# Kernel tuning notes

Hardware: AMD Instinct MI355X
Metric: run time of the kernel (lower is better)

The kernel has to match this reference:

```python
import jax, jax.numpy as jnp
import numpy as np

N_ENTS = 50000
N_RELS = 500
EMB = 256
N_LAYERS = 2
N_EDGES = 400000
BATCH = 512
BN_EPS = 1e-5


def make_quaternion_mul(kernel):
    # kernel: [m, 4*dim] -> hamilton: [4*m, 4*dim]
    r, i, j, k = jnp.split(kernel, 4, axis=1)
    r2 = jnp.concatenate([r, -i, -j, -k], axis=0)
    i2 = jnp.concatenate([i, r, -k, j], axis=0)
    j2 = jnp.concatenate([j, k, r, -i], axis=0)
    k2 = jnp.concatenate([k, -j, i, r], axis=0)
    return jnp.concatenate([r2, i2, j2, k2], axis=1)


def batchnorm(x, gamma, beta):
    mean = jnp.mean(x, axis=0)
    var = jnp.var(x, axis=0)  # biased, as torch BN training normalization
    return (x - mean) * jax.lax.rsqrt(var + BN_EPS) * gamma + beta


def q4gnn_layer(X, rows, cols, vals, W, gamma, beta, n_nodes):
    hamilton = make_quaternion_mul(W)          # [d, d]
    support = X @ hamilton                     # [n, d]
    agg = jax.ops.segment_sum(vals[:, None] * support[cols], rows, num_segments=n_nodes)
    return jnp.tanh(batchnorm(agg, gamma, beta))


def vec_vec_wise_multiplication(q, p):
    # quaternion componentwise-normalized hamilton product; q, p: [B, d]
    d = q.shape[1]
    size = d // 4
    pn = p.reshape(-1, 4, size)
    pn = pn / jnp.sqrt(jnp.sum(pn * pn, axis=1, keepdims=True))
    pn = pn.reshape(-1, d)
    qr, qi, qj, qk = jnp.split(q, 4, axis=1)
    q_r = jnp.concatenate([qr, -qi, -qj, -qk], axis=1)
    q_i = jnp.concatenate([qi, qr, -qk, qj], axis=1)
    q_j = jnp.concatenate([qj, qk, qr, -qi], axis=1)
    q_k = jnp.concatenate([qk, -qj, qi, qr], axis=1)
    def qwise(x):
        return jnp.sum((x * pn).reshape(-1, 4, size), axis=1)
    return jnp.concatenate([qwise(q_r), qwise(q_i), qwise(q_j), qwise(q_k)], axis=1)


def quate_score(h, r, X, gamma, beta):
    hr = vec_vec_wise_multiplication(h, r)
    hr = batchnorm(hr, gamma, beta)            # dropout = identity (eval)
    return hr @ X.T                            # [B, n_ents]


def setup_inputs() -> dict:
    key = jax.random.key(0)
    ks = jax.random.split(key, 12)
    return {
        "e1_idx": jax.random.randint(ks[0], (BATCH,), 0, N_ENTS),
        "r_idx": jax.random.randint(ks[1], (BATCH,), 0, N_RELS),
        "embeddings": jax.random.normal(ks[2], (N_ENTS + N_RELS, EMB), jnp.float32) * 0.1,
        "gcn1_w": jax.random.normal(ks[3], (N_LAYERS, EMB // 4, EMB), jnp.float32) * 0.1,
        "gcn2_w": jax.random.normal(ks[4], (N_LAYERS, EMB // 4, EMB), jnp.float32) * 0.1,
        "gcn1_gamma": jnp.ones((N_LAYERS, EMB), jnp.float32),
        "gcn1_beta": jnp.zeros((N_LAYERS, EMB), jnp.float32),
        "gcn2_gamma": jnp.ones((N_LAYERS, EMB), jnp.float32),
        "gcn2_beta": jnp.zeros((N_LAYERS, EMB), jnp.float32),
        "lin_ents": jax.random.normal(ks[5], (N_LAYERS, EMB // 2, EMB), jnp.float32) * 0.1,
        "bn_s_gamma": jnp.ones((3, EMB), jnp.float32),
        "bn_s_beta": jnp.zeros((3, EMB), jnp.float32),
        "adj_rows": jax.random.randint(ks[6], (N_EDGES,), 0, N_ENTS),
        "adj_cols": jax.random.randint(ks[7], (N_EDGES,), 0, N_ENTS),
        "adj_vals": jax.random.uniform(ks[8], (N_EDGES,), jnp.float32),
        "adjr_rows": jax.random.randint(ks[9], (N_EDGES,), 0, N_ENTS + N_RELS),
        "adjr_cols": jax.random.randint(ks[10], (N_EDGES,), 0, N_ENTS + N_RELS),
        "adjr_vals": jax.random.uniform(ks[11], (N_EDGES,), jnp.float32),
    }


def reference(e1_idx, r_idx, embeddings, gcn1_w, gcn2_w, gcn1_gamma, gcn1_beta,
              gcn2_gamma, gcn2_beta, lin_ents, bn_s_gamma, bn_s_beta,
              adj_rows, adj_cols, adj_vals, adjr_rows, adjr_cols, adjr_vals):
    X = embeddings[:N_ENTS]
    R = embeddings[N_ENTS:]
    scores = [jax.nn.sigmoid(quate_score(X[e1_idx], R[r_idx], X, bn_s_gamma[0], bn_s_beta[0]))]
    for l in range(N_LAYERS):
        XR = jnp.concatenate([X, R], axis=0)
        XRrf = q4gnn_layer(XR, adjr_rows, adjr_cols, adjr_vals,
                           gcn2_w[l], gcn2_gamma[l], gcn2_beta[l], N_ENTS + N_RELS)
        Xef = q4gnn_layer(X, adj_rows, adj_cols, adj_vals,
                          gcn1_w[l], gcn1_gamma[l], gcn1_beta[l], N_ENTS)
        Xrf = XRrf[:N_ENTS]
        # combine_type == 'cat': interleave quaternion components -> [N, 2*EMB]
        e1, e2, e3, e4 = jnp.split(Xef, 4, axis=1)
        r1, r2, r3, r4 = jnp.split(Xrf, 4, axis=1)
        Xcat = jnp.concatenate([e1, r1, e2, r2, e3, r3, e4, r4], axis=1)
        X = Xcat @ make_quaternion_mul(lin_ents[l])  # [N, EMB]
        R = XRrf[N_ENTS:]
        scores.append(jax.nn.sigmoid(
            quate_score(X[e1_idx], R[r_idx], X, bn_s_gamma[l + 1], bn_s_beta[l + 1])))
    return jnp.stack(scores)  # [N_LAYERS+1, B, N_ENTS]
```

## Files before the change

kernel.cpp:

```cpp
#include <hip/hip_runtime.h>
#include <math.h>

#define N_ENTS 50000
#define N_RELS 500
#define N_ALL  50500
#define EMB    256
#define NEDGE  400000
#define BATCH  512
#define BN_EPS 1e-5f

typedef unsigned short u16;
typedef unsigned int   u32;
typedef __attribute__((ext_vector_type(8))) short s16x8;
typedef __attribute__((ext_vector_type(4))) float f32x4;

#define LSTR 40

__device__ __forceinline__ u16 f2b(float x) {
    u32 u = __float_as_uint(x);
    return (u16)((u + 0x7fffu + ((u >> 16) & 1u)) >> 16);
}
__device__ __forceinline__ float b2f(u16 h) {
    return __uint_as_float((u32)h << 16);
}

__global__ __launch_bounds__(256) void split_kernel(
    const float* __restrict__ x, u16* __restrict__ hi, u16* __restrict__ lo,
    long n4) {
    long i = (long)blockIdx.x * 256 + threadIdx.x;
    if (i >= n4) return;
    float4 v = ((const float4*)x)[i];
    u16 h0 = f2b(v.x), h1 = f2b(v.y), h2 = f2b(v.z), h3 = f2b(v.w);
    u16 l0 = f2b(v.x - b2f(h0)), l1 = f2b(v.y - b2f(h1));
    u16 l2 = f2b(v.z - b2f(h2)), l3 = f2b(v.w - b2f(h3));
    uint2 hp, lp;
    hp.x = (u32)h0 | ((u32)h1 << 16); hp.y = (u32)h2 | ((u32)h3 << 16);
    lp.x = (u32)l0 | ((u32)l1 << 16); lp.y = (u32)l2 | ((u32)l3 << 16);
    ((uint2*)hi)[i] = hp;
    ((uint2*)lo)[i] = lp;
}

__global__ __launch_bounds__(256) void build_ht_kernel(
    const float* __restrict__ W, u16* __restrict__ Hhi, u16* __restrict__ Hlo,
    int P) {
    int K4 = 4 * P;
    int idx = blockIdx.x * 256 + threadIdx.x;
    int total = 256 * K4;
    if (idx >= total) return;
    int n = idx / K4, k = idx - n * K4;
    int a = k / P, p = k - a * P;
    int c = n >> 6, s = n & 63;
    const int  comp[4][4] = {{0,1,2,3},{1,0,3,2},{2,3,0,1},{3,2,1,0}};
    const float sgn[4][4] = {{1.f,1.f,1.f,1.f},
                             {-1.f,1.f,1.f,-1.f},
                             {-1.f,-1.f,1.f,1.f},
                             {-1.f,1.f,-1.f,1.f}};
    float v = sgn[a][c] * W[p * 256 + comp[a][c] * 64 + s];
    u16 h = f2b(v);
    Hhi[idx] = h;
    Hlo[idx] = f2b(v - b2f(h));
}

__global__ __launch_bounds__(256) void bn_coeff_kernel(
    const float* __restrict__ stats, int n, const float* __restrict__ gamma,
    const float* __restrict__ beta, float2* __restrict__ coef) {
    int col = threadIdx.x;
    float inv_n = 1.f / (float)n;
    float mean = stats[col] * inv_n;
    float var = stats[256 + col] * inv_n - mean * mean;
    float sc = rsqrtf(var + BN_EPS) * gamma[col];
    coef[col] = make_float2(sc, beta[col] - mean * sc);
}

template <int ROWS>
__device__ __forceinline__ void stage_rows(
    const u16* __restrict__ Shi, const u16* __restrict__ Slo,
    long row0, int rows_left, int K, int k0,
    u16* __restrict__ Lh, u16* __restrict__ Ll, int tid) {
#pragma unroll
    for (int p = 0; p < ROWS / 64; p++) {
        int idx = tid + p * 256;
        int r = idx >> 2, c = idx & 3;
        uint4 vh = make_uint4(0, 0, 0, 0), vl = make_uint4(0, 0, 0, 0);
        if (r < rows_left) {
            long base = (row0 + r) * (long)K + k0 + c * 8;
            vh = *(const uint4*)&Shi[base];
            vl = *(const uint4*)&Slo[base];
        }
        *(uint4*)&Lh[r * LSTR + c * 8] = vh;
        *(uint4*)&Ll[r * LSTR + c * 8] = vl;
    }
}

__device__ __forceinline__ void stage_f32_split(
    const float* __restrict__ S, long row0, int rows_left, int K, int k0,
    u16* __restrict__ Lh, u16* __restrict__ Ll, int tid) {
#pragma unroll
    for (int p = 0; p < 4; p++) {
        int idx = tid + p * 256;
        int r = idx >> 3, c4 = idx & 7;
        float4 v = make_float4(0.f, 0.f, 0.f, 0.f);
        if (r < rows_left)
            v = *(const float4*)&S[(row0 + r) * (long)K + k0 + c4 * 4];
        u16 h0 = f2b(v.x), h1 = f2b(v.y), h2 = f2b(v.z), h3 = f2b(v.w);
        u16 l0 = f2b(v.x - b2f(h0)), l1 = f2b(v.y - b2f(h1));
        u16 l2 = f2b(v.z - b2f(h2)), l3 = f2b(v.w - b2f(h3));
        uint2 hp, lp;
        hp.x = (u32)h0 | ((u32)h1 << 16); hp.y = (u32)h2 | ((u32)h3 << 16);
        lp.x = (u32)l0 | ((u32)l1 << 16); lp.y = (u32)l2 | ((u32)l3 << 16);
        *(uint2*)&Lh[r * LSTR + c4 * 4] = hp;
        *(uint2*)&Ll[r * LSTR + c4 * 4] = lp;
    }
}

__device__ __forceinline__ void mfma_tile256(
    const u16* __restrict__ Ah, const u16* __restrict__ Al,
    const u16* __restrict__ Bh, const u16* __restrict__ Bl,
    int wm, int wn, int lane, f32x4 acc[4][8]) {
    int lr = lane & 15, kg = lane >> 4;
    s16x8 ah[4], al[4];
#pragma unroll
    for (int fm = 0; fm < 4; fm++) {
        int off = (wm + fm * 16 + lr) * LSTR + kg * 8;
        ah[fm] = *(const s16x8*)&Ah[off];
        al[fm] = *(const s16x8*)&Al[off];
    }
#pragma unroll
    for (int fn = 0; fn < 8; fn++) {
        int off = (wn + fn * 16 + lr) * LSTR + kg * 8;
        s16x8 bh = *(const s16x8*)&Bh[off];
        s16x8 bl = *(const s16x8*)&Bl[off];
#pragma unroll
        for (int fm = 0; fm < 4; fm++) {
            acc[fm][fn] = __builtin_amdgcn_mfma_f32_16x16x32_bf16(
                ah[fm], bh, acc[fm][fn], 0, 0, 0);
            acc[fm][fn] = __builtin_amdgcn_mfma_f32_16x16x32_bf16(
                ah[fm], bl, acc[fm][fn], 0, 0, 0);
            acc[fm][fn] = __builtin_amdgcn_mfma_f32_16x16x32_bf16(
                al[fm], bh, acc[fm][fn], 0, 0, 0);
        }
    }
}

__global__ __launch_bounds__(256, 2) void mfma_agg_kernel(
    const float* __restrict__ G,
    const u16* __restrict__ Bhi, const u16* __restrict__ Blo,
    float* __restrict__ C, float* __restrict__ stats, int M) {
    __shared__ u16 Ah[128 * LSTR], Al[128 * LSTR];
    __shared__ u16 Bh[256 * LSTR], Bl[256 * LSTR];
    int tid = threadIdx.x, lane = tid & 63, wid = tid >> 6;
    int wm = (wid >> 1) * 64, wn = (wid & 1) * 128;
    long bm0 = (long)blockIdx.y * 128;
    int rA = (int)(((long)M - bm0 < 128) ? (long)M - bm0 : 128);
    f32x4 acc[4][8] = {};
    for (int k0 = 0; k0 < 256; k0 += 32) {
        if (k0) __syncthreads();
        stage_f32_split(G, bm0, rA, 256, k0, Ah, Al, tid);
        stage_rows<256>(Bhi, Blo, 0, 256, 256, k0, Bh, Bl, tid);
        __syncthreads();
        mfma_tile256(Ah, Al, Bh, Bl, wm, wn, lane, acc);
    }
    int lr = lane & 15, lq = lane >> 4;
#pragma unroll
    for (int fm = 0; fm < 4; fm++) {
#pragma unroll
        for (int r = 0; r < 4; r++) {
            long row = bm0 + wm + fm * 16 + lq * 4 + r;
            if (row < M) {
#pragma unroll
                for (int fn = 0; fn < 8; fn++) {
                    long col = wn + fn * 16 + lr;
                    C[row * 256 + col] = acc[fm][fn][r];
                }
            }
        }
    }
#pragma unroll
    for (int fn = 0; fn < 8; fn++) {
        float s = 0.f, sq = 0.f;
#pragma unroll
        for (int fm = 0; fm < 4; fm++)
#pragma unroll
            for (int r = 0; r < 4; r++) {
                float v = acc[fm][fn][r];
                s += v;
                sq += v * v;
            }
        s += __shfl_xor(s, 16);  s += __shfl_xor(s, 32);
        sq += __shfl_xor(sq, 16); sq += __shfl_xor(sq, 32);
        if (lane < 16) {
            int col = wn + fn * 16 + lr;
            atomicAdd(&stats[col], s);
            atomicAdd(&stats[256 + col], sq);
        }
    }
}

__global__ __launch_bounds__(256, 2) void mfma_score_kernel(
    const u16* __restrict__ Ahi, const u16* __restrict__ Alo,
    const u16* __restrict__ Bhi, const u16* __restrict__ Blo,
    float* __restrict__ out) {
    __shared__ u16 Ah[128 * LSTR], Al[128 * LSTR];
    __shared__ u16 Bh[256 * LSTR], Bl[256 * LSTR];
    int tid = threadIdx.x, lane = tid & 63, wid = tid >> 6;
    int wm = (wid >> 1) * 64, wn = (wid & 1) * 128;
    long bm0 = (long)blockIdx.y * 128, bn0 = (long)blockIdx.x * 256;
    int rB = (int)(((long)N_ENTS - bn0 < 256) ? (long)N_ENTS - bn0 : 256);
    f32x4 acc[4][8] = {};
    for (int k0 = 0; k0 < 256; k0 += 32) {
        if (k0) __syncthreads();
        stage_rows<128>(Ahi, Alo, bm0, 128, 256, k0, Ah, Al, tid);
        stage_rows<256>(Bhi, Blo, bn0, rB, 256, k0, Bh, Bl, tid);
        __syncthreads();
        mfma_tile256(Ah, Al, Bh, Bl, wm, wn, lane, acc);
    }
    int lr = lane & 15, lq = lane >> 4;
#pragma unroll
    for (int fm = 0; fm < 4; fm++) {
#pragma unroll
        for (int r = 0; r < 4; r++) {
            long row = bm0 + wm + fm * 16 + lq * 4 + r;
#pragma unroll
            for (int fn = 0; fn < 8; fn++) {
                long col = bn0 + wn + fn * 16 + lr;
                if (col < N_ENTS) {
                    float v = acc[fm][fn][r];
                    out[row * N_ENTS + col] = 1.f / (1.f + __expf(-v));
                }
            }
        }
    }
}

__global__ __launch_bounds__(256, 2) void mfma_lin_kernel(
    const float* __restrict__ Xef, const float* __restrict__ Xrf,
    const float2* __restrict__ coefE, const float2* __restrict__ coefR,
    const u16* __restrict__ Bhi, const u16* __restrict__ Blo,
    u16* __restrict__ Chi, u16* __restrict__ Clo, int M) {
    __shared__ u16 Ah[128 * LSTR], Al[128 * LSTR];
    __shared__ u16 Bh[256 * LSTR], Bl[256 * LSTR];
    int tid = threadIdx.x, lane = tid & 63, wid = tid >> 6;
    int wm = (wid >> 1) * 64, wn = (wid & 1) * 128;
    int bm0 = blockIdx.y * 128;
    f32x4 acc[4][8] = {};
    for (int k0 = 0; k0 < 512; k0 += 32) {
        if (k0) __syncthreads();
#pragma unroll
        for (int p = 0; p < 4; p++) {
            int idx = tid + p * 256;
            int r = idx >> 3, c4 = idx & 7;
            int kk = k0 + c4 * 4;
            int chunk = kk >> 6, s = kk & 63;
            int gm = bm0 + r;
            const float* src = (chunk & 1) ? Xrf : Xef;
            const float2* cf = (chunk & 1) ? coefR : coefE;
            int base = (chunk >> 1) * 64 + s;
            float4 v = make_float4(0.f, 0.f, 0.f, 0.f);
            if (gm < M) v = *(const float4*)&src[(long)gm * 256 + base];
            float2 c0 = cf[base], c1 = cf[base + 1];
            float2 c2 = cf[base + 2], c3 = cf[base + 3];
            v.x = tanhf(fmaf(v.x, c0.x, c0.y));
            v.y = tanhf(fmaf(v.y, c1.x, c1.y));
            v.z = tanhf(fmaf(v.z, c2.x, c2.y));
            v.w = tanhf(fmaf(v.w, c3.x, c3.y));
            u16 h0 = f2b(v.x), h1 = f2b(v.y), h2 = f2b(v.z), h3 = f2b(v.w);
            u16 l0 = f2b(v.x - b2f(h0)), l1 = f2b(v.y - b2f(h1));
            u16 l2 = f2b(v.z - b2f(h2)), l3 = f2b(v.w - b2f(h3));
            uint2 hp, lp;
            hp.x = (u32)h0 | ((u32)h1 << 16); hp.y = (u32)h2 | ((u32)h3 << 16);
            lp.x = (u32)l0 | ((u32)l1 << 16); lp.y = (u32)l2 | ((u32)l3 << 16);
            *(uint2*)&Ah[r * LSTR + c4 * 4] = hp;
            *(uint2*)&Al[r * LSTR + c4 * 4] = lp;
        }
        stage_rows<256>(Bhi, Blo, 0, 256, 512, k0, Bh, Bl, tid);
        __syncthreads();
        mfma_tile256(Ah, Al, Bh, Bl, wm, wn, lane, acc);
    }
    int lr = lane & 15, lq = lane >> 4;
#pragma unroll
    for (int fm = 0; fm < 4; fm++) {
#pragma unroll
        for (int r = 0; r < 4; r++) {
            long row = (long)bm0 + wm + fm * 16 + lq * 4 + r;
            if (row < M) {
#pragma unroll
                for (int fn = 0; fn < 8; fn++) {
                    long col = wn + fn * 16 + lr;
                    float v = acc[fm][fn][r];
                    u16 h = f2b(v);
                    Chi[row * 256 + col] = h;
                    Clo[row * 256 + col] = f2b(v - b2f(h));
                }
            }
        }
    }
}

__global__ __launch_bounds__(256) void hist_kernel(
    const int* __restrict__ rows, int* __restrict__ cnt, int n_edges) {
    int e = blockIdx.x * 256 + threadIdx.x;
    if (e < n_edges) atomicAdd(&cnt[rows[e]], 1);
}

__global__ __launch_bounds__(1024) void exscan_kernel(
    const int* __restrict__ cnt, int n, int* __restrict__ off) {
    __shared__ int part[1024];
    int t = threadIdx.x;
    int chunk = (n + 1023) / 1024;
    int lo = t * chunk;
    int hi = lo + chunk; if (hi > n) hi = n;
    int s = 0;
    for (int i = lo; i < hi; i++) s += cnt[i];
    part[t] = s;
    __syncthreads();
    for (int d = 1; d < 1024; d <<= 1) {
        int v = (t >= d) ? part[t - d] : 0;
        __syncthreads();
        part[t] += v;
        __syncthreads();
    }
    int base = (t == 0) ? 0 : part[t - 1];
    for (int i = lo; i < hi; i++) {
        off[i] = base;
        base += cnt[i];
    }
    if (hi >= n) off[n] = base;
}

__global__ __launch_bounds__(256) void scatter_kernel(
    const int* __restrict__ rows, const int* __restrict__ cols,
    const float* __restrict__ vals, int* __restrict__ cursor,
    int2* __restrict__ pack, int n_edges) {
    int e = blockIdx.x * 256 + threadIdx.x;
    if (e >= n_edges) return;
    int r = rows[e];
    int p = atomicAdd(&cursor[r], 1);
    pack[p] = make_int2(cols[e], __float_as_int(vals[e]));
}

__global__ __launch_bounds__(256) void csr_gather_kernel(
    const u16* __restrict__ xhi, const u16* __restrict__ xlo,
    const int* __restrict__ off, const int2* __restrict__ pack,
    float* __restrict__ G, int n_rows) {
    int gid = blockIdx.x * 256 + threadIdx.x;
    int row = gid >> 6;
    int lane = gid & 63;
    if (row >= n_rows) return;
    int beg = off[row], end = off[row + 1];
    float4 acc = {0.f, 0.f, 0.f, 0.f};
    int e = beg;
    for (; e + 4 <= end; e += 4) {
        int2 cv0 = pack[e], cv1 = pack[e + 1], cv2 = pack[e + 2], cv3 = pack[e + 3];
        long b0 = (long)cv0.x * 256 + lane * 4;
        long b1 = (long)cv1.x * 256 + lane * 4;
        long b2 = (long)cv2.x * 256 + lane * 4;
        long b3 = (long)cv3.x * 256 + lane * 4;
        uint2 h0 = *(const uint2*)(xhi + b0), l0 = *(const uint2*)(xlo + b0);
        uint2 h1 = *(const uint2*)(xhi + b1), l1 = *(const uint2*)(xlo + b1);
        uint2 h2 = *(const uint2*)(xhi + b2), l2 = *(const uint2*)(xlo + b2);
        uint2 h3 = *(const uint2*)(xhi + b3), l3 = *(const uint2*)(xlo + b3);
        float v0 = __int_as_float(cv0.y), v1 = __int_as_float(cv1.y);
        float v2 = __int_as_float(cv2.y), v3 = __int_as_float(cv3.y);
        acc.x = fmaf(v0, b2f((u16)(h0.x & 0xffff)) + b2f((u16)(l0.x & 0xffff)), acc.x);
        acc.y = fmaf(v0, b2f((u16)(h0.x >> 16))    + b2f((u16)(l0.x >> 16)),    acc.y);
        acc.z = fmaf(v0, b2f((u16)(h0.y & 0xffff)) + b2f((u16)(l0.y & 0xffff)), acc.z);
        acc.w = fmaf(v0, b2f((u16)(h0.y >> 16))    + b2f((u16)(l0.y >> 16)),    acc.w);
        acc.x = fmaf(v1, b2f((u16)(h1.x & 0xffff)) + b2f((u16)(l1.x & 0xffff)), acc.x);
        acc.y = fmaf(v1, b2f((u16)(h1.x >> 16))    + b2f((u16)(l1.x >> 16)),    acc.y);
        acc.z = fmaf(v1, b2f((u16)(h1.y & 0xffff)) + b2f((u16)(l1.y & 0xffff)), acc.z);
        acc.w = fmaf(v1, b2f((u16)(h1.y >> 16))    + b2f((u16)(l1.y >> 16)),    acc.w);
        acc.x = fmaf(v2, b2f((u16)(h2.x & 0xffff)) + b2f((u16)(l2.x & 0xffff)), acc.x);
        acc.y = fmaf(v2, b2f((u16)(h2.x >> 16))    + b2f((u16)(l2.x >> 16)),    acc.y);
        acc.z = fmaf(v2, b2f((u16)(h2.y & 0xffff)) + b2f((u16)(l2.y & 0xffff)), acc.z);
        acc.w = fmaf(v2, b2f((u16)(h2.y >> 16))    + b2f((u16)(l2.y >> 16)),    acc.w);
        acc.x = fmaf(v3, b2f((u16)(h3.x & 0xffff)) + b2f((u16)(l3.x & 0xffff)), acc.x);
        acc.y = fmaf(v3, b2f((u16)(h3.x >> 16))    + b2f((u16)(l3.x >> 16)),    acc.y);
        acc.z = fmaf(v3, b2f((u16)(h3.y & 0xffff)) + b2f((u16)(l3.y & 0xffff)), acc.z);
        acc.w = fmaf(v3, b2f((u16)(h3.y >> 16))    + b2f((u16)(l3.y >> 16)),    acc.w);
    }
    for (; e < end; e++) {
        int2 cv = pack[e];
        float v = __int_as_float(cv.y);
        long b = (long)cv.x * 256 + lane * 4;
        uint2 hv = *(const uint2*)(xhi + b), lv = *(const uint2*)(xlo + b);
        acc.x = fmaf(v, b2f((u16)(hv.x & 0xffff)) + b2f((u16)(lv.x & 0xffff)), acc.x);
        acc.y = fmaf(v, b2f((u16)(hv.x >> 16))    + b2f((u16)(lv.x >> 16)),    acc.y);
        acc.z = fmaf(v, b2f((u16)(hv.y & 0xffff)) + b2f((u16)(lv.y & 0xffff)), acc.z);
        acc.w = fmaf(v, b2f((u16)(hv.y >> 16))    + b2f((u16)(lv.y >> 16)),    acc.w);
    }
    *(float4*)(G + (long)row * 256 + lane * 4) = acc;
}

__global__ __launch_bounds__(256) void bn_stats_kernel(
    const float* __restrict__ x, int n, float* __restrict__ stats) {
    int col = threadIdx.x;
    int r0 = blockIdx.x * 256;
    int r1 = r0 + 256;
    if (r1 > n) r1 = n;
    float s = 0.f, sq = 0.f;
    for (int r = r0; r < r1; r++) {
        float v = x[(long)r * 256 + col];
        s += v;
        sq += v * v;
    }
    atomicAdd(&stats[col], s);
    atomicAdd(&stats[256 + col], sq);
}

__global__ __launch_bounds__(256) void bn_apply_split_kernel(
    const float* __restrict__ x, u16* __restrict__ hi, u16* __restrict__ lo,
    int n, const float* __restrict__ gamma, const float* __restrict__ beta,
    const float* __restrict__ stats) {
    long total = (long)n * 256;
    float inv_n = 1.f / (float)n;
    long idx = (long)blockIdx.x * 256 + threadIdx.x;
    if (idx >= total) return;
    int col = (int)(idx & 255);
    float mean = stats[col] * inv_n;
    float var = stats[256 + col] * inv_n - mean * mean;
    float sc = rsqrtf(var + BN_EPS) * gamma[col];
    float v = (x[idx] - mean) * sc + beta[col];
    u16 h = f2b(v);
    hi[idx] = h;
    lo[idx] = f2b(v - b2f(h));
}

__global__ __launch_bounds__(256) void bn_tanh_split_kernel(
    const float* __restrict__ x, const float2* __restrict__ coef,
    u16* __restrict__ hi, u16* __restrict__ lo, long total) {
    long idx = (long)blockIdx.x * 256 + threadIdx.x;
    if (idx >= total) return;
    int col = (int)(idx & 255);
    float2 c = coef[col];
    float v = tanhf(fmaf(x[idx], c.x, c.y));
    u16 h = f2b(v);
    hi[idx] = h;
    lo[idx] = f2b(v - b2f(h));
}

__global__ __launch_bounds__(256) void hr_kernel(
    const u16* __restrict__ xhi, const u16* __restrict__ xlo,
    const int* __restrict__ e1_idx, const int* __restrict__ r_idx,
    float* __restrict__ hr) {
    int idx = blockIdx.x * 256 + threadIdx.x;
    if (idx >= BATCH * 64) return;
    int b = idx >> 6, s = idx & 63;
    long hrow = (long)e1_idx[b] * 256;
    long prow = ((long)N_ENTS + r_idx[b]) * 256;
    float qr = b2f(xhi[hrow + s])       + b2f(xlo[hrow + s]);
    float qi = b2f(xhi[hrow + 64 + s])  + b2f(xlo[hrow + 64 + s]);
    float qj = b2f(xhi[hrow + 128 + s]) + b2f(xlo[hrow + 128 + s]);
    float qk = b2f(xhi[hrow + 192 + s]) + b2f(xlo[hrow + 192 + s]);
    float pr = b2f(xhi[prow + s])       + b2f(xlo[prow + s]);
    float pi = b2f(xhi[prow + 64 + s])  + b2f(xlo[prow + 64 + s]);
    float pj = b2f(xhi[prow + 128 + s]) + b2f(xlo[prow + 128 + s]);
    float pk = b2f(xhi[prow + 192 + s]) + b2f(xlo[prow + 192 + s]);
    float inv = rsqrtf(pr * pr + pi * pi + pj * pj + pk * pk);
    pr *= inv; pi *= inv; pj *= inv; pk *= inv;
    float* o = hr + (long)b * 256 + s;
    o[0]   = qr * pr - qi * pi - qj * pj - qk * pk;
    o[64]  = qi * pr + qr * pi - qk * pj + qj * pk;
    o[128] = qj * pr + qk * pi + qr * pj - qi * pk;
    o[192] = qk * pr - qj * pi + qi * pj + qr * pk;
}

struct Csr {
    int* off;
    int* cur;
    int2* pack;
};

struct Ws {
    float* Gbuf;
    float* aggA;
    float* aggB;
    float* hr;
    float* statsHr;
    float* statsA;
    float* statsB;
    float2* coefA;
    float2* coefB;
    u16* xr_hi;
    u16* xr_lo;
    u16* hrn_hi;
    u16* hrn_lo;
    u16* ht_hi;
    u16* ht_lo;
    Csr adj;
    Csr adjr;
};

static void build_csr(const int* rows, const int* cols, const float* vals,
                      int n_rows, const Csr& c, hipStream_t stream) {
    hipMemsetAsync(c.cur, 0, (size_t)n_rows * sizeof(int), stream);
    hist_kernel<<<(NEDGE + 255) / 256, 256, 0, stream>>>(rows, c.cur, NEDGE);
    exscan_kernel<<<1, 1024, 0, stream>>>(c.cur, n_rows, c.off);
    hipMemcpyAsync(c.cur, c.off, (size_t)n_rows * sizeof(int),
                   hipMemcpyDeviceToDevice, stream);
    scatter_kernel<<<(NEDGE + 255) / 256, 256, 0, stream>>>(
        rows, cols, vals, c.cur, c.pack, NEDGE);
}

static void run_split(const float* x, u16* hi, u16* lo, long n,
                      hipStream_t stream) {
    long n4 = n / 4;
    split_kernel<<<(int)((n4 + 255) / 256), 256, 0, stream>>>(x, hi, lo, n4);
}

static void run_q4gnn(int n, const Csr& c, const float* W,
                      const float* gamma, const float* beta,
                      float* agg, float* stats, float2* coef,
                      const Ws& w, hipStream_t stream) {
    hipMemsetAsync(stats, 0, 512 * sizeof(float), stream);
    int gblocks = (n * 64 + 255) / 256;
    csr_gather_kernel<<<gblocks, 256, 0, stream>>>(
        w.xr_hi, w.xr_lo, c.off, c.pack, w.Gbuf, n);
    build_ht_kernel<<<(256 * 256) / 256, 256, 0, stream>>>(W, w.ht_hi, w.ht_lo, 64);
    dim3 g(1, (n + 127) / 128);
    mfma_agg_kernel<<<g, 256, 0, stream>>>(w.Gbuf, w.ht_hi, w.ht_lo, agg, stats, n);
    bn_coeff_kernel<<<1, 256, 0, stream>>>(stats, n, gamma, beta, coef);
}

static void run_score(const int* e1_idx, const int* r_idx, const float* gamma,
                      const float* beta, float* out_l, const Ws& w,
                      hipStream_t stream) {
    hr_kernel<<<(BATCH * 64) / 256, 256, 0, stream>>>(
        w.xr_hi, w.xr_lo, e1_idx, r_idx, w.hr);
    hipMemsetAsync(w.statsHr, 0, 512 * sizeof(float), stream);
    bn_stats_kernel<<<(BATCH + 255) / 256, 256, 0, stream>>>(w.hr, BATCH, w.statsHr);
    bn_apply_split_kernel<<<(BATCH * 256) / 256, 256, 0, stream>>>(
        w.hr, w.hrn_hi, w.hrn_lo, BATCH, gamma, beta, w.statsHr);
    dim3 g((N_ENTS + 255) / 256, BATCH / 128);
    mfma_score_kernel<<<g, 256, 0, stream>>>(
        w.hrn_hi, w.hrn_lo, w.xr_hi, w.xr_lo, out_l);
}

extern "C" void kernel_launch(void* const* d_in, const int* in_sizes, int n_in,
                              void* d_out, int out_size, void* d_ws, size_t ws_size,
                              hipStream_t stream) {
    const int*   e1_idx     = (const int*)d_in[0];
    const int*   r_idx      = (const int*)d_in[1];
    const float* emb        = (const float*)d_in[2];
    const float* gcn1_w     = (const float*)d_in[3];
    const float* gcn2_w     = (const float*)d_in[4];
    const float* gcn1_gamma = (const float*)d_in[5];
    const float* gcn1_beta  = (const float*)d_in[6];
    const float* gcn2_gamma = (const float*)d_in[7];
    const float* gcn2_beta  = (const float*)d_in[8];
    const float* lin_ents   = (const float*)d_in[9];
    const float* bn_s_gamma = (const float*)d_in[10];
    const float* bn_s_beta  = (const float*)d_in[11];
    const int*   adj_rows   = (const int*)d_in[12];
    const int*   adj_cols   = (const int*)d_in[13];
    const float* adj_vals   = (const float*)d_in[14];
    const int*   adjr_rows  = (const int*)d_in[15];
    const int*   adjr_cols  = (const int*)d_in[16];
    const float* adjr_vals  = (const float*)d_in[17];
    float* out = (float*)d_out;

    Ws w;
    float* f = (float*)d_ws;
    w.Gbuf       = f; f += (long)N_ALL * EMB;
    w.aggA       = f; f += (long)N_ALL * EMB;
    w.aggB       = f; f += (long)N_ENTS * EMB;
    w.hr         = f; f += BATCH * EMB;
    w.statsHr    = f; f += 512;
    w.statsA     = f; f += 512;
    w.statsB     = f; f += 512;
    w.coefA      = (float2*)f; f += 512;
    w.coefB      = (float2*)f; f += 512;
    w.xr_hi  = (u16*)f; f += (long)N_ALL * EMB / 2;
    w.xr_lo  = (u16*)f; f += (long)N_ALL * EMB / 2;
    w.hrn_hi = (u16*)f; f += BATCH * EMB / 2;
    w.hrn_lo = (u16*)f; f += BATCH * EMB / 2;
    w.ht_hi  = (u16*)f; f += 256 * 512 / 2;
    w.ht_lo  = (u16*)f; f += 256 * 512 / 2;
    int* ip = (int*)f;
    w.adj.pack  = (int2*)ip; ip += 2 * NEDGE;
    w.adjr.pack = (int2*)ip; ip += 2 * NEDGE;
    w.adj.off    = ip; ip += N_ENTS + 1;
    w.adj.cur    = ip; ip += N_ENTS;
    w.adjr.off   = ip; ip += N_ALL + 1;
    w.adjr.cur   = ip; ip += N_ALL;

    build_csr(adj_rows, adj_cols, adj_vals, N_ENTS, w.adj, stream);
    build_csr(adjr_rows, adjr_cols, adjr_vals, N_ALL, w.adjr, stream);

    run_split(emb, w.xr_hi, w.xr_lo, (long)N_ALL * EMB, stream);

    run_score(e1_idx, r_idx, bn_s_gamma, bn_s_beta, out, w, stream);

    for (int l = 0; l < 2; l++) {
        run_q4gnn(N_ALL, w.adjr, gcn2_w + (long)l * 64 * 256,
                  gcn2_gamma + l * 256, gcn2_beta + l * 256,
                  w.aggA, w.statsA, w.coefA, w, stream);
        run_q4gnn(N_ENTS, w.adj, gcn1_w + (long)l * 64 * 256,
                  gcn1_gamma + l * 256, gcn1_beta + l * 256,
                  w.aggB, w.statsB, w.coefB, w, stream);
        build_ht_kernel<<<(256 * 512) / 256, 256, 0, stream>>>(
            lin_ents + (long)l * 128 * 256, w.ht_hi, w.ht_lo, 128);
        dim3 g(1, (N_ENTS + 127) / 128);
        mfma_lin_kernel<<<g, 256, 0, stream>>>(
            w.aggB, w.aggA, w.coefB, w.coefA, w.ht_hi, w.ht_lo,
            w.xr_hi, w.xr_lo, N_ENTS);
        bn_tanh_split_kernel<<<(N_RELS * EMB + 255) / 256, 256, 0, stream>>>(
            w.aggA + (long)N_ENTS * EMB, w.coefA,
            w.xr_hi + (long)N_ENTS * EMB, w.xr_lo + (long)N_ENTS * EMB,
            (long)N_RELS * EMB);
        run_score(e1_idx, r_idx, bn_s_gamma + (l + 1) * 256,
                  bn_s_beta + (l + 1) * 256,
                  out + (long)(l + 1) * BATCH * N_ENTS, w, stream);
    }
}
```

Measured before the change: 1.667 ms.

## Batch both GNN branches into shared gather/GEMM launches and remap score blocks

The two q4gnn branches (relation graph and entity graph) now run their CSR gathers in one combined launch and their Hamilton GEMMs in one combined launch, with separate gather buffers and Hamilton matrices so neither branch overwrites the other. This cuts the number of launches and fills the GPU better, especially for the small tail grids. The score GEMM now uses a 1D grid whose block index is remapped so that consecutive blocks spread across groups of eight, which changes which blocks run together and which B tiles they share in cache. It costs an extra gather buffer and one more Hamilton buffer in workspace.

After: 1.634 ms. 1.02x faster.

```diff
diff --git a/kernel.cpp b/kernel.cpp
--- a/kernel.cpp
+++ b/kernel.cpp
@@ -142,21 +142,32 @@
     }
 }
 
-__global__ __launch_bounds__(256, 2) void mfma_agg_kernel(
-    const float* __restrict__ G,
-    const u16* __restrict__ Bhi, const u16* __restrict__ Blo,
-    float* __restrict__ C, float* __restrict__ stats, int M) {
+__global__ __launch_bounds__(256, 2) void mfma_agg2_kernel(
+    const float* __restrict__ GA, const float* __restrict__ GB,
+    const u16* __restrict__ AhiB, const u16* __restrict__ AloB,
+    const u16* __restrict__ BhiB, const u16* __restrict__ BloB,
+    float* __restrict__ CA, float* __restrict__ CB,
+    float* __restrict__ statsA, float* __restrict__ statsB, int tA) {
     __shared__ u16 Ah[128 * LSTR], Al[128 * LSTR];
     __shared__ u16 Bh[256 * LSTR], Bl[256 * LSTR];
     int tid = threadIdx.x, lane = tid & 63, wid = tid >> 6;
     int wm = (wid >> 1) * 64, wn = (wid & 1) * 128;
-    long bm0 = (long)blockIdx.y * 128;
+    int by = blockIdx.y;
+    const float* G; const u16* Hhi; const u16* Hlo;
+    float* C; float* stats; int M; long bm0;
+    if (by < tA) {
+        G = GA; Hhi = AhiB; Hlo = AloB; C = CA; stats = statsA;
+        M = N_ALL; bm0 = (long)by * 128;
+    } else {
+        G = GB; Hhi = BhiB; Hlo = BloB; C = CB; stats = statsB;
+        M = N_ENTS; bm0 = (long)(by - tA) * 128;
+    }
     int rA = (int)(((long)M - bm0 < 128) ? (long)M - bm0 : 128);
     f32x4 acc[4][8] = {};
     for (int k0 = 0; k0 < 256; k0 += 32) {
         if (k0) __syncthreads();
         stage_f32_split(G, bm0, rA, 256, k0, Ah, Al, tid);
-        stage_rows<256>(Bhi, Blo, 0, 256, 256, k0, Bh, Bl, tid);
+        stage_rows<256>(Hhi, Hlo, 0, 256, 256, k0, Bh, Bl, tid);
         __syncthreads();
         mfma_tile256(Ah, Al, Bh, Bl, wm, wn, lane, acc);
     }
@@ -204,7 +215,10 @@
     __shared__ u16 Bh[256 * LSTR], Bl[256 * LSTR];
     int tid = threadIdx.x, lane = tid & 63, wid = tid >> 6;
     int wm = (wid >> 1) * 64, wn = (wid & 1) * 128;
-    long bm0 = (long)blockIdx.y * 128, bn0 = (long)blockIdx.x * 256;
+    int b = blockIdx.x;
+    int w = (b & 7) * 98 + (b >> 3);
+    long bm0 = (long)(w & 3) * 128;
+    long bn0 = (long)(w >> 2) * 256;
     int rB = (int)(((long)N_ENTS - bn0 < 256) ? (long)N_ENTS - bn0 : 256);
     f32x4 acc[4][8] = {};
     for (int k0 = 0; k0 < 256; k0 += 32) {
@@ -338,15 +352,23 @@
     pack[p] = make_int2(cols[e], __float_as_int(vals[e]));
 }
 
-__global__ __launch_bounds__(256) void csr_gather_kernel(
+__global__ __launch_bounds__(256) void csr_gather2_kernel(
     const u16* __restrict__ xhi, const u16* __restrict__ xlo,
-    const int* __restrict__ off, const int2* __restrict__ pack,
-    float* __restrict__ G, int n_rows) {
+    const int* __restrict__ offA, const int2* __restrict__ packA,
+    const int* __restrict__ offB, const int2* __restrict__ packB,
+    float* __restrict__ GA, float* __restrict__ GB, int nA, int nB) {
     int gid = blockIdx.x * 256 + threadIdx.x;
     int row = gid >> 6;
     int lane = gid & 63;
-    if (row >= n_rows) return;
-    int beg = off[row], end = off[row + 1];
+    const int* off; const int2* pack; float* G; int r;
+    if (row < nA) {
+        off = offA; pack = packA; G = GA; r = row;
+    } else {
+        r = row - nA;
+        if (r >= nB) return;
+        off = offB; pack = packB; G = GB;
+    }
+    int beg = off[r], end = off[r + 1];
     float4 acc = {0.f, 0.f, 0.f, 0.f};
     int e = beg;
     for (; e + 4 <= end; e += 4) {
@@ -388,7 +410,7 @@
         acc.z = fmaf(v, b2f((u16)(hv.y & 0xffff)) + b2f((u16)(lv.y & 0xffff)), acc.z);
         acc.w = fmaf(v, b2f((u16)(hv.y >> 16))    + b2f((u16)(lv.y >> 16)),    acc.w);
     }
-    *(float4*)(G + (long)row * 256 + lane * 4) = acc;
+    *(float4*)(G + (long)r * 256 + lane * 4) = acc;
 }
 
 __global__ __launch_bounds__(256) void bn_stats_kernel(
@@ -471,7 +493,8 @@
 };
 
 struct Ws {
-    float* Gbuf;
+    float* GA;
+    float* GB;
     float* aggA;
     float* aggB;
     float* hr;
@@ -486,6 +509,8 @@
     u16* hrn_lo;
     u16* ht_hi;
     u16* ht_lo;
+    u16* ht1_hi;
+    u16* ht1_lo;
     Csr adj;
     Csr adjr;
 };
@@ -507,20 +532,6 @@
     split_kernel<<<(int)((n4 + 255) / 256), 256, 0, stream>>>(x, hi, lo, n4);
 }
 
-static void run_q4gnn(int n, const Csr& c, const float* W,
-                      const float* gamma, const float* beta,
-                      float* agg, float* stats, float2* coef,
-                      const Ws& w, hipStream_t stream) {
-    hipMemsetAsync(stats, 0, 512 * sizeof(float), stream);
-    int gblocks = (n * 64 + 255) / 256;
-    csr_gather_kernel<<<gblocks, 256, 0, stream>>>(
-        w.xr_hi, w.xr_lo, c.off, c.pack, w.Gbuf, n);
-    build_ht_kernel<<<(256 * 256) / 256, 256, 0, stream>>>(W, w.ht_hi, w.ht_lo, 64);
-    dim3 g(1, (n + 127) / 128);
-    mfma_agg_kernel<<<g, 256, 0, stream>>>(w.Gbuf, w.ht_hi, w.ht_lo, agg, stats, n);
-    bn_coeff_kernel<<<1, 256, 0, stream>>>(stats, n, gamma, beta, coef);
-}
-
 static void run_score(const int* e1_idx, const int* r_idx, const float* gamma,
                       const float* beta, float* out_l, const Ws& w,
                       hipStream_t stream) {
@@ -530,8 +541,7 @@
     bn_stats_kernel<<<(BATCH + 255) / 256, 256, 0, stream>>>(w.hr, BATCH, w.statsHr);
     bn_apply_split_kernel<<<(BATCH * 256) / 256, 256, 0, stream>>>(
         w.hr, w.hrn_hi, w.hrn_lo, BATCH, gamma, beta, w.statsHr);
-    dim3 g((N_ENTS + 255) / 256, BATCH / 128);
-    mfma_score_kernel<<<g, 256, 0, stream>>>(
+    mfma_score_kernel<<<784, 256, 0, stream>>>(
         w.hrn_hi, w.hrn_lo, w.xr_hi, w.xr_lo, out_l);
 }
 
@@ -560,7 +570,8 @@
 
     Ws w;
     float* f = (float*)d_ws;
-    w.Gbuf       = f; f += (long)N_ALL * EMB;
+    w.GA         = f; f += (long)N_ALL * EMB;
+    w.GB         = f; f += (long)N_ENTS * EMB;
     w.aggA       = f; f += (long)N_ALL * EMB;
     w.aggB       = f; f += (long)N_ENTS * EMB;
     w.hr         = f; f += BATCH * EMB;
@@ -575,6 +586,8 @@
     w.hrn_lo = (u16*)f; f += BATCH * EMB / 2;
     w.ht_hi  = (u16*)f; f += 256 * 512 / 2;
     w.ht_lo  = (u16*)f; f += 256 * 512 / 2;
+    w.ht1_hi = (u16*)f; f += 256 * 256 / 2;
+    w.ht1_lo = (u16*)f; f += 256 * 256 / 2;
     int* ip = (int*)f;
     w.adj.pack  = (int2*)ip; ip += 2 * NEDGE;
     w.adjr.pack = (int2*)ip; ip += 2 * NEDGE;
@@ -590,13 +603,28 @@
 
     run_score(e1_idx, r_idx, bn_s_gamma, bn_s_beta, out, w, stream);
 
+    const int tA = (N_ALL + 127) / 128;
+    const int tB = (N_ENTS + 127) / 128;
+
     for (int l = 0; l < 2; l++) {
-        run_q4gnn(N_ALL, w.adjr, gcn2_w + (long)l * 64 * 256,
-                  gcn2_gamma + l * 256, gcn2_beta + l * 256,
-                  w.aggA, w.statsA, w.coefA, w, stream);
-        run_q4gnn(N_ENTS, w.adj, gcn1_w + (long)l * 64 * 256,
-                  gcn1_gamma + l * 256, gcn1_beta + l * 256,
-                  w.aggB, w.statsB, w.coefB, w, stream);
+        hipMemsetAsync(w.statsA, 0, 512 * sizeof(float), stream);
+        hipMemsetAsync(w.statsB, 0, 512 * sizeof(float), stream);
+        build_ht_kernel<<<(256 * 256) / 256, 256, 0, stream>>>(
+            gcn2_w + (long)l * 64 * 256, w.ht_hi, w.ht_lo, 64);
+        build_ht_kernel<<<(256 * 256) / 256, 256, 0, stream>>>(
+            gcn1_w + (long)l * 64 * 256, w.ht1_hi, w.ht1_lo, 64);
+        int grows = N_ALL + N_ENTS;
+        csr_gather2_kernel<<<(grows * 64 + 255) / 256, 256, 0, stream>>>(
+            w.xr_hi, w.xr_lo, w.adjr.off, w.adjr.pack, w.adj.off, w.adj.pack,
+            w.GA, w.GB, N_ALL, N_ENTS);
+        dim3 g2(1, tA + tB);
+        mfma_agg2_kernel<<<g2, 256, 0, stream>>>(
+            w.GA, w.GB, w.ht_hi, w.ht_lo, w.ht1_hi, w.ht1_lo,
+            w.aggA, w.aggB, w.statsA, w.statsB, tA);
+        bn_coeff_kernel<<<1, 256, 0, stream>>>(
+            w.statsA, N_ALL, gcn2_gamma + l * 256, gcn2_beta + l * 256, w.coefA);
+        bn_coeff_kernel<<<1, 256, 0, stream>>>(
+            w.statsB, N_ENTS, gcn1_gamma + l * 256, gcn1_beta + l * 256, w.coefB);
         build_ht_kernel<<<(256 * 512) / 256, 256, 0, stream>>>(
             lin_ents + (long)l * 128 * 256, w.ht_hi, w.ht_lo, 128);
         dim3 g(1, (N_ENTS + 127) / 128);
```
